# Optimization experiments

Hardware: AMD Instinct MI355X
Metric: run time of the kernel (lower is better)

The kernel has to match this reference:

```python
import jax, jax.numpy as jnp
import numpy as np

PAD_IDX = 1
BATCH = 16
TLEN = 128
SLEN = 400          # full source length
AGENDA_LEN = 100    # slen_ in src_map
CONTEXT_LEN = SLEN - AGENDA_LEN
INPUT_SIZE = 1024
VOCAB = 32000
CVOCAB = 120


def setup_inputs() -> dict:
    key = jax.random.key(0)
    k1, k2, k3, k4, k5, k6, k7 = jax.random.split(key, 7)
    N = BATCH * TLEN
    hidden = jax.random.normal(k1, (N, INPUT_SIZE), dtype=jnp.float32)
    attn = jax.random.uniform(k2, (N, SLEN), dtype=jnp.float32)
    attn = attn / jnp.sum(attn, axis=1, keepdims=True)  # attention-like rows
    src_map = jax.random.uniform(k3, (AGENDA_LEN, BATCH, CVOCAB), dtype=jnp.float32)
    W = jax.random.normal(k4, (VOCAB, INPUT_SIZE), dtype=jnp.float32) * 0.02
    b = jnp.zeros((VOCAB,), dtype=jnp.float32)
    W_copy = jax.random.normal(k5, (1, INPUT_SIZE), dtype=jnp.float32) * 0.02
    b_copy = jnp.zeros((1,), dtype=jnp.float32)
    return {"hidden": hidden, "attn": attn, "src_map": src_map,
            "W": W, "b": b, "W_copy": W_copy, "b_copy": b_copy}


def reference(hidden, attn, src_map, W, b, W_copy, b_copy):
    # hidden: (tlen*batch, d), attn: (tlen*batch, slen), src_map: (agenda, batch, cvocab)
    agenda_len, batch, cvocab = src_map.shape
    slen = attn.shape[1]
    context_len = slen - agenda_len

    logits = hidden @ W.T + b                       # (N, vocab)
    logits = logits.at[:, PAD_IDX].set(-jnp.inf)
    prob = jax.nn.softmax(logits, axis=1)
    p_copy = jax.nn.sigmoid(hidden @ W_copy.T + b_copy)  # (N, 1)

    out_prob = prob * (1.0 - p_copy)                # (N, vocab)
    mul_attn = attn[:, context_len:] * p_copy       # (N, agenda)

    # rows are ordered (tlen, batch); bmm against per-batch indicator map
    ma = mul_attn.reshape(-1, batch, agenda_len)    # (tlen, batch, agenda)
    copy_prob = jnp.einsum('tba,abv->tbv', ma, src_map)  # (tlen, batch, cvocab)
    copy_prob = copy_prob.reshape(-1, cvocab)       # (N, cvocab)

    return jnp.concatenate([out_prob, copy_prob], axis=1), p_copy
```

## Files before the change

### kernel.cpp

```cpp
#include <hip/hip_runtime.h>

#define M_DIM 2048
#define K_DIM 1024
#define N_DIM 32000
#define CVOCAB 120
#define AGENDA 100
#define SLEN 400
#define CTX 300
#define BATCH 16
#define OUT_STRIDE 32120
#define PAD_IDX 1

#define TM 256
#define TN 256
#define BK 64
#define BUFSZ (TM * BK)
#define NKT (K_DIM / BK)
#define MT (M_DIM / TM)
#define NT (N_DIM / TN)

typedef float f32x4_t  __attribute__((ext_vector_type(4)));
typedef __bf16 bf16x8_t __attribute__((ext_vector_type(8)));
typedef unsigned short u16x8_t __attribute__((ext_vector_type(8)));
typedef unsigned short u16x4_t __attribute__((ext_vector_type(4)));

__device__ __forceinline__ unsigned short f2bf(float f) {
    union { float f; unsigned int u; } c; c.f = f;
    unsigned int u = c.u;
    u += 0x7FFFu + ((u >> 16) & 1u);
    return (unsigned short)(u >> 16);
}

__device__ __forceinline__ unsigned short f2h(float f) {
    _Float16 h = (_Float16)f;
    unsigned short u; __builtin_memcpy(&u, &h, 2); return u;
}
__device__ __forceinline__ float h2f(unsigned short u) {
    _Float16 h; __builtin_memcpy(&h, &u, 2); return (float)h;
}

__device__ __forceinline__ void async_copy16(const void* gsrc, void* ldst) {
    __builtin_amdgcn_global_load_lds(
        (__attribute__((address_space(1))) unsigned int*)(gsrc),
        (__attribute__((address_space(3))) unsigned int*)(ldst),
        16, 0, 0);
}

__global__ void cast_bf16_kernel(const float4* __restrict__ W, const float4* __restrict__ H,
                                 unsigned short* __restrict__ Wb, unsigned short* __restrict__ Hb) {
    const size_t NW4 = (size_t)N_DIM * K_DIM / 4;
    const size_t NH4 = (size_t)M_DIM * K_DIM / 4;
    size_t idx = (size_t)blockIdx.x * 256 + threadIdx.x;
    float4 v; unsigned short* dst;
    if (idx < NW4)            { v = W[idx];        dst = Wb + idx * 4; }
    else if (idx < NW4 + NH4) { v = H[idx - NW4];  dst = Hb + (idx - NW4) * 4; }
    else return;
    u16x4_t o;
    o[0] = f2bf(v.x); o[1] = f2bf(v.y); o[2] = f2bf(v.z); o[3] = f2bf(v.w);
    *(u16x4_t*)dst = o;
}

__global__ void pcopy_kernel(const float* __restrict__ hidden, const float* __restrict__ Wc,
                             const float* __restrict__ bc, float* __restrict__ pcopy,
                             float* __restrict__ rowsum) {
    int row  = blockIdx.x * 4 + (threadIdx.x >> 6);
    int lane = threadIdx.x & 63;
    const float4* h = (const float4*)(hidden + (size_t)row * K_DIM);
    const float4* w = (const float4*)Wc;
    float s = 0.f;
    #pragma unroll
    for (int i = 0; i < 4; ++i) {
        float4 a = h[lane + 64 * i];
        float4 b = w[lane + 64 * i];
        s += a.x * b.x + a.y * b.y + a.z * b.z + a.w * b.w;
    }
    #pragma unroll
    for (int m = 1; m < 64; m <<= 1) s += __shfl_xor(s, m);
    if (lane == 0) {
        float p = 1.0f / (1.0f + __expf(-(s + bc[0])));
        pcopy[row] = p;
        rowsum[row] = 0.0f;
    }
}

__global__ __launch_bounds__(1024, 4) void gemm_exp_kernel(
    const unsigned short* __restrict__ A,
    const unsigned short* __restrict__ B,
    const float* __restrict__ bias,
    float* __restrict__ out,
    float* __restrict__ rowsum)
{
    __shared__ unsigned short sA[2][BUFSZ];
    __shared__ unsigned short sB[2][BUFSZ];
    __shared__ float sRow[TM];

    const int tid   = threadIdx.x;
    const int lane  = tid & 63;
    const int q     = lane >> 4;
    const int lr    = lane & 15;
    const int wv    = tid >> 6;
    const int waveM = wv >> 2;
    const int waveN = wv & 3;

    const int bid = blockIdx.x;
    const int t   = (bid & 7) * NT + (bid >> 3);
    const int rowBase = (t & 7) * TM;
    const int colBase = (t >> 3) * TN;

    f32x4_t acc[4][4] = {};
    if (tid < TM) sRow[tid] = 0.0f;

    const int p0 = tid,        m0 = p0 >> 3, j0 = (p0 & 7) ^ (m0 & 7);
    const int p1 = 1024 + tid, m1 = p1 >> 3, j1 = (p1 & 7) ^ (m1 & 7);
    const unsigned short* aSrc0 = A + (size_t)(rowBase + m0) * K_DIM + j0 * 8;
    const unsigned short* aSrc1 = A + (size_t)(rowBase + m1) * K_DIM + j1 * 8;
    const unsigned short* bSrc0 = B + (size_t)(colBase + m0) * K_DIM + j0 * 8;
    const unsigned short* bSrc1 = B + (size_t)(colBase + m1) * K_DIM + j1 * 8;
    const int dOff0 = (tid & ~63) * 8;
    const int dOff1 = (1024 + (tid & ~63)) * 8;

    async_copy16(aSrc0, &sA[0][dOff0]);
    async_copy16(aSrc1, &sA[0][dOff1]);
    async_copy16(bSrc0, &sB[0][dOff0]);
    async_copy16(bSrc1, &sB[0][dOff1]);
    __syncthreads();

    for (int kt = 0; kt < NKT; ++kt) {
        const int cur = kt & 1;
        if (kt + 1 < NKT) {
            const int nb = cur ^ 1;
            const int k0 = (kt + 1) * BK;
            async_copy16(aSrc0 + k0, &sA[nb][dOff0]);
            async_copy16(aSrc1 + k0, &sA[nb][dOff1]);
            async_copy16(bSrc0 + k0, &sB[nb][dOff0]);
            async_copy16(bSrc1 + k0, &sB[nb][dOff1]);
        }
        const unsigned short* pA = sA[cur];
        const unsigned short* pB = sB[cur];
        #pragma unroll
        for (int s = 0; s < 2; ++s) {
            u16x8_t af[4], bfr[4];
            #pragma unroll
            for (int r = 0; r < 4; ++r) {
                int m  = waveM * 64 + r * 16 + lr;
                int ch = (s * 4 + q) ^ (m & 7);
                af[r] = *(const u16x8_t*)(pA + m * BK + ch * 8);
            }
            #pragma unroll
            for (int c = 0; c < 4; ++c) {
                int n  = waveN * 64 + c * 16 + lr;
                int ch = (s * 4 + q) ^ (n & 7);
                bfr[c] = *(const u16x8_t*)(pB + n * BK + ch * 8);
            }
            #pragma unroll
            for (int r = 0; r < 4; ++r)
                #pragma unroll
                for (int c = 0; c < 4; ++c)
                    acc[r][c] = __builtin_amdgcn_mfma_f32_16x16x32_bf16(
                        __builtin_bit_cast(bf16x8_t, af[r]),
                        __builtin_bit_cast(bf16x8_t, bfr[c]),
                        acc[r][c], 0, 0, 0);
        }
        __syncthreads();
    }

    float bb[4];
    #pragma unroll
    for (int c = 0; c < 4; ++c) bb[c] = bias[colBase + waveN * 64 + c * 16 + lr];

    #pragma unroll
    for (int r = 0; r < 4; ++r) {
        float rsum[4] = {0.f, 0.f, 0.f, 0.f};
        #pragma unroll
        for (int c = 0; c < 4; ++c) {
            int gcol = colBase + waveN * 64 + c * 16 + lr;
            bool pad = (gcol == PAD_IDX);
            #pragma unroll
            for (int d = 0; d < 4; ++d) {
                int grow = rowBase + waveM * 64 + r * 16 + q * 4 + d;
                float e = pad ? 0.0f : __expf(acc[r][c][d] + bb[c]);
                ((unsigned short*)(out + (size_t)grow * OUT_STRIDE))[gcol] = f2h(e);
                rsum[d] += e;
            }
        }
        #pragma unroll
        for (int d = 0; d < 4; ++d) {
            float v = rsum[d];
            v += __shfl_xor(v, 1);
            v += __shfl_xor(v, 2);
            v += __shfl_xor(v, 4);
            v += __shfl_xor(v, 8);
            if (lr == 0) {
                int lrow = waveM * 64 + r * 16 + q * 4 + d;
                atomicAdd(&sRow[lrow], v);
            }
        }
    }
    __syncthreads();
    if (tid < TM) atomicAdd(&rowsum[rowBase + tid], sRow[tid]);
}

__global__ __launch_bounds__(512) void finalize_kernel(
    float* __restrict__ out, const float* __restrict__ rowsum,
    const float* __restrict__ pcopy, const float* __restrict__ attn,
    const float* __restrict__ src_map, float* __restrict__ out_tail) {
    const int n   = blockIdx.x;
    const int tid = threadIdx.x;
    __shared__ unsigned short sE[N_DIM];
    __shared__ float ma[AGENDA];

    const float p = pcopy[n];
    const float scale = (1.0f - p) / rowsum[n];

    const u16x8_t* src = (const u16x8_t*)(out + (size_t)n * OUT_STRIDE);
    for (int j = tid; j < N_DIM / 8; j += 512)
        *(u16x8_t*)(sE + j * 8) = src[j];
    if (tid < AGENDA) ma[tid] = attn[(size_t)n * SLEN + CTX + tid] * p;
    __syncthreads();

    float4* row4 = (float4*)(out + (size_t)n * OUT_STRIDE);
    for (int j = tid; j < N_DIM / 4; j += 512) {
        u16x4_t h = *(const u16x4_t*)(sE + j * 4);
        float4 v;
        v.x = h2f(h[0]) * scale;
        v.y = h2f(h[1]) * scale;
        v.z = h2f(h[2]) * scale;
        v.w = h2f(h[3]) * scale;
        row4[j] = v;
    }

    if (tid < CVOCAB) {
        int bidx = n & (BATCH - 1);
        float s = 0.f;
        #pragma unroll 4
        for (int a = 0; a < AGENDA; ++a)
            s += ma[a] * src_map[(size_t)(a * BATCH + bidx) * CVOCAB + tid];
        out[(size_t)n * OUT_STRIDE + N_DIM + tid] = s;
    }
    if (tid == 0) out_tail[n] = p;
}

extern "C" void kernel_launch(void* const* d_in, const int* in_sizes, int n_in,
                              void* d_out, int out_size, void* d_ws, size_t ws_size,
                              hipStream_t stream) {
    const float* hidden  = (const float*)d_in[0];
    const float* attn    = (const float*)d_in[1];
    const float* src_map = (const float*)d_in[2];
    const float* W       = (const float*)d_in[3];
    const float* b       = (const float*)d_in[4];
    const float* W_copy  = (const float*)d_in[5];
    const float* b_copy  = (const float*)d_in[6];
    float* out = (float*)d_out;

    char* ws = (char*)d_ws;
    unsigned short* Wb = (unsigned short*)ws;
    unsigned short* Hb = (unsigned short*)(ws + 65536000);
    float* rowsum      = (float*)(ws + 65536000 + 4194304);
    float* pcopy       = (float*)(ws + 65536000 + 4194304 + 8192);

    float* out_tail = out + (size_t)M_DIM * OUT_STRIDE;

    {
        size_t total4 = (size_t)N_DIM * K_DIM / 4 + (size_t)M_DIM * K_DIM / 4;
        int blocks = (int)((total4 + 255) / 256);
        cast_bf16_kernel<<<blocks, 256, 0, stream>>>((const float4*)W, (const float4*)hidden, Wb, Hb);
    }
    pcopy_kernel<<<M_DIM / 4, 256, 0, stream>>>(hidden, W_copy, b_copy, pcopy, rowsum);
    gemm_exp_kernel<<<MT * NT, 1024, 0, stream>>>(Hb, Wb, b, out, rowsum);
    finalize_kernel<<<M_DIM, 512, 0, stream>>>(out, rowsum, pcopy, attn, src_map, out_tail);
}
```

Before: 582.8 us.

## Restructure GEMM main loop into 8-wave ping-pong schedule with deeper prefetch

The GEMM block drops from 16 waves to 8. Each wave now computes a 128x64 sub-tile with 32 accumulators, which raises register reuse of the B fragments. The K loop is split into half-K stages across a 4-buffer LDS ring (128KB) with two-stage-ahead async prefetch. Explicit vmcnt waits, s_barrier phases, sched_barrier and setprio interleave the loads with the MFMA bursts. The larger LDS footprint and register pressure may limit occupancy to one block per CU, and the many barriers add synchronisation cost.

```diff
diff --git a/kernel.cpp b/kernel.cpp
--- a/kernel.cpp
+++ b/kernel.cpp
@@ -14,7 +14,6 @@
 #define TM 256
 #define TN 256
 #define BK 64
-#define BUFSZ (TM * BK)
 #define NKT (K_DIM / BK)
 #define MT (M_DIM / TM)
 #define NT (N_DIM / TN)
@@ -83,102 +82,135 @@
     }
 }
 
-__global__ __launch_bounds__(1024, 4) void gemm_exp_kernel(
+__global__ __launch_bounds__(512, 2) void gemm_exp_kernel(
     const unsigned short* __restrict__ A,
     const unsigned short* __restrict__ B,
     const float* __restrict__ bias,
     float* __restrict__ out,
     float* __restrict__ rowsum)
 {
-    __shared__ unsigned short sA[2][BUFSZ];
-    __shared__ unsigned short sB[2][BUFSZ];
+    __shared__ unsigned short lds[65536];
     __shared__ float sRow[TM];
 
-    const int tid   = threadIdx.x;
-    const int lane  = tid & 63;
-    const int q     = lane >> 4;
-    const int lr    = lane & 15;
-    const int wv    = tid >> 6;
-    const int waveM = wv >> 2;
-    const int waveN = wv & 3;
+    const int tid  = threadIdx.x;
+    const int lane = tid & 63;
+    const int q    = lane >> 4;
+    const int lr   = lane & 15;
+    const int wv   = tid >> 6;
+    const int wr   = wv >> 2;
+    const int wc   = wv & 3;
 
     const int bid = blockIdx.x;
-    const int t   = (bid & 7) * NT + (bid >> 3);
-    const int rowBase = (t & 7) * TM;
-    const int colBase = (t >> 3) * TN;
-
-    f32x4_t acc[4][4] = {};
+    const int t0  = (bid & 7) * NT + (bid >> 3);
+    const int rowBase = (t0 & 7) * TM;
+    const int colBase = (t0 >> 3) * TN;
+
     if (tid < TM) sRow[tid] = 0.0f;
 
-    const int p0 = tid,        m0 = p0 >> 3, j0 = (p0 & 7) ^ (m0 & 7);
-    const int p1 = 1024 + tid, m1 = p1 >> 3, j1 = (p1 & 7) ^ (m1 & 7);
-    const unsigned short* aSrc0 = A + (size_t)(rowBase + m0) * K_DIM + j0 * 8;
-    const unsigned short* aSrc1 = A + (size_t)(rowBase + m1) * K_DIM + j1 * 8;
-    const unsigned short* bSrc0 = B + (size_t)(colBase + m0) * K_DIM + j0 * 8;
-    const unsigned short* bSrc1 = B + (size_t)(colBase + m1) * K_DIM + j1 * 8;
-    const int dOff0 = (tid & ~63) * 8;
-    const int dOff1 = (1024 + (tid & ~63)) * 8;
-
-    async_copy16(aSrc0, &sA[0][dOff0]);
-    async_copy16(aSrc1, &sA[0][dOff1]);
-    async_copy16(bSrc0, &sB[0][dOff0]);
-    async_copy16(bSrc1, &sB[0][dOff1]);
-    __syncthreads();
-
-    for (int kt = 0; kt < NKT; ++kt) {
-        const int cur = kt & 1;
-        if (kt + 1 < NKT) {
-            const int nb = cur ^ 1;
-            const int k0 = (kt + 1) * BK;
-            async_copy16(aSrc0 + k0, &sA[nb][dOff0]);
-            async_copy16(aSrc1 + k0, &sA[nb][dOff1]);
-            async_copy16(bSrc0 + k0, &sB[nb][dOff0]);
-            async_copy16(bSrc1 + k0, &sB[nb][dOff1]);
-        }
-        const unsigned short* pA = sA[cur];
-        const unsigned short* pB = sB[cur];
-        #pragma unroll
-        for (int s = 0; s < 2; ++s) {
-            u16x8_t af[4], bfr[4];
-            #pragma unroll
-            for (int r = 0; r < 4; ++r) {
-                int m  = waveM * 64 + r * 16 + lr;
-                int ch = (s * 4 + q) ^ (m & 7);
-                af[r] = *(const u16x8_t*)(pA + m * BK + ch * 8);
-            }
-            #pragma unroll
-            for (int c = 0; c < 4; ++c) {
-                int n  = waveN * 64 + c * 16 + lr;
-                int ch = (s * 4 + q) ^ (n & 7);
-                bfr[c] = *(const u16x8_t*)(pB + n * BK + ch * 8);
-            }
-            #pragma unroll
-            for (int r = 0; r < 4; ++r)
-                #pragma unroll
-                for (int c = 0; c < 4; ++c)
-                    acc[r][c] = __builtin_amdgcn_mfma_f32_16x16x32_bf16(
-                        __builtin_bit_cast(bf16x8_t, af[r]),
-                        __builtin_bit_cast(bf16x8_t, bfr[c]),
-                        acc[r][c], 0, 0, 0);
-        }
-        __syncthreads();
-    }
+    const int mS0 = tid >> 2,         cS0 = tid & 3;
+    const int mS1 = (tid + 512) >> 2, cS1 = tid & 3;
+    const int jS0 = cS0 ^ ((mS0 >> 1) & 3);
+    const int jS1 = cS1 ^ ((mS1 >> 1) & 3);
+    const unsigned short* aS0 = A + (size_t)(rowBase + mS0) * K_DIM + jS0 * 8;
+    const unsigned short* aS1 = A + (size_t)(rowBase + mS1) * K_DIM + jS1 * 8;
+    const unsigned short* bS0 = B + (size_t)(colBase + mS0) * K_DIM + jS0 * 8;
+    const unsigned short* bS1 = B + (size_t)(colBase + mS1) * K_DIM + jS1 * 8;
+    const int dus0 = wv * 512;
+    const int dus1 = 4096 + wv * 512;
+
+    int aoff[8], boff[4];
+    #pragma unroll
+    for (int f = 0; f < 8; ++f) {
+        int m = wr * 128 + f * 16 + lr;
+        aoff[f] = m * 32 + ((q ^ ((m >> 1) & 3)) * 8);
+    }
+    #pragma unroll
+    for (int c = 0; c < 4; ++c) {
+        int n = wc * 64 + c * 16 + lr;
+        boff[c] = n * 32 + ((q ^ ((n >> 1) & 3)) * 8);
+    }
+
+    f32x4_t acc[8][4] = {};
+
+#define STAGE_A(TT, S) do {                                                  \
+    unsigned short* d_ = lds + (((TT) & 1) * 2 + (S)) * 8192;                \
+    const size_t ko_ = (size_t)(TT) * 64 + (S) * 32;                         \
+    async_copy16(aS0 + ko_, d_ + dus0);                                      \
+    async_copy16(aS1 + ko_, d_ + dus1); } while (0)
+
+#define STAGE_B(TT, S) do {                                                  \
+    unsigned short* d_ = lds + 32768 + (((TT) & 1) * 2 + (S)) * 8192;        \
+    const size_t ko_ = (size_t)(TT) * 64 + (S) * 32;                         \
+    async_copy16(bS0 + ko_, d_ + dus0);                                      \
+    async_copy16(bS1 + ko_, d_ + dus1); } while (0)
+
+    STAGE_A(0, 0); STAGE_B(0, 0);
+    STAGE_A(0, 1); STAGE_B(0, 1);
+    STAGE_A(1, 0); STAGE_B(1, 0);
+
+    #pragma unroll 1
+    for (int t = 0; t < NKT; ++t) {
+        const int p = t & 1;
+        if (t < NKT - 1) asm volatile("s_waitcnt vmcnt(4)" ::: "memory");
+        else             asm volatile("s_waitcnt vmcnt(0)" ::: "memory");
+        __builtin_amdgcn_s_barrier();
+        __builtin_amdgcn_sched_barrier(0);
+
+        u16x8_t bfv[4];
+
+#define PHASE(MH, S, STAGE_STMT) do {                                        \
+        const int sa_ = (p * 2 + (S)) * 8192;                                \
+        const int sb_ = 32768 + sa_;                                         \
+        u16x8_t af_[4];                                                      \
+        _Pragma("unroll")                                                    \
+        for (int r = 0; r < 4; ++r)                                          \
+            af_[r] = *(const u16x8_t*)(lds + sa_ + aoff[(MH) * 4 + r]);      \
+        if ((MH) == 0) {                                                     \
+            _Pragma("unroll")                                                \
+            for (int c = 0; c < 4; ++c)                                      \
+                bfv[c] = *(const u16x8_t*)(lds + sb_ + boff[c]);             \
+        }                                                                    \
+        STAGE_STMT;                                                          \
+        __builtin_amdgcn_sched_barrier(0);                                   \
+        __builtin_amdgcn_s_barrier();                                        \
+        __builtin_amdgcn_s_setprio(1);                                       \
+        _Pragma("unroll")                                                    \
+        for (int r = 0; r < 4; ++r) {                                        \
+            _Pragma("unroll")                                                \
+            for (int c = 0; c < 4; ++c)                                      \
+                acc[(MH) * 4 + r][c] = __builtin_amdgcn_mfma_f32_16x16x32_bf16( \
+                    __builtin_bit_cast(bf16x8_t, af_[r]),                    \
+                    __builtin_bit_cast(bf16x8_t, bfv[c]),                    \
+                    acc[(MH) * 4 + r][c], 0, 0, 0);                          \
+        }                                                                    \
+        __builtin_amdgcn_s_setprio(0);                                       \
+        __builtin_amdgcn_sched_barrier(0);                                   \
+        __builtin_amdgcn_s_barrier(); } while (0)
+
+        PHASE(0, 0, { if (t < NKT - 1) STAGE_A(t + 1, 1); });
+        PHASE(1, 0, { if (t < NKT - 1) STAGE_B(t + 1, 1); });
+        PHASE(0, 1, { if (t < NKT - 2) STAGE_A(t + 2, 0); });
+        PHASE(1, 1, { if (t < NKT - 2) STAGE_B(t + 2, 0); });
+#undef PHASE
+    }
+#undef STAGE_A
+#undef STAGE_B
 
     float bb[4];
     #pragma unroll
-    for (int c = 0; c < 4; ++c) bb[c] = bias[colBase + waveN * 64 + c * 16 + lr];
-
-    #pragma unroll
-    for (int r = 0; r < 4; ++r) {
+    for (int c = 0; c < 4; ++c) bb[c] = bias[colBase + wc * 64 + c * 16 + lr];
+
+    #pragma unroll
+    for (int f = 0; f < 8; ++f) {
         float rsum[4] = {0.f, 0.f, 0.f, 0.f};
         #pragma unroll
         for (int c = 0; c < 4; ++c) {
-            int gcol = colBase + waveN * 64 + c * 16 + lr;
+            int gcol = colBase + wc * 64 + c * 16 + lr;
             bool pad = (gcol == PAD_IDX);
             #pragma unroll
             for (int d = 0; d < 4; ++d) {
-                int grow = rowBase + waveM * 64 + r * 16 + q * 4 + d;
-                float e = pad ? 0.0f : __expf(acc[r][c][d] + bb[c]);
+                int grow = rowBase + wr * 128 + f * 16 + q * 4 + d;
+                float e = pad ? 0.0f : __expf(acc[f][c][d] + bb[c]);
                 ((unsigned short*)(out + (size_t)grow * OUT_STRIDE))[gcol] = f2h(e);
                 rsum[d] += e;
             }
@@ -191,7 +223,7 @@
             v += __shfl_xor(v, 4);
             v += __shfl_xor(v, 8);
             if (lr == 0) {
-                int lrow = waveM * 64 + r * 16 + q * 4 + d;
+                int lrow = wr * 128 + f * 16 + q * 4 + d;
                 atomicAdd(&sRow[lrow], v);
             }
         }
@@ -266,6 +298,6 @@
         cast_bf16_kernel<<<blocks, 256, 0, stream>>>((const float4*)W, (const float4*)hidden, Wb, Hb);
     }
     pcopy_kernel<<<M_DIM / 4, 256, 0, stream>>>(hidden, W_copy, b_copy, pcopy, rowsum);
-    gemm_exp_kernel<<<MT * NT, 1024, 0, stream>>>(Hb, Wb, b, out, rowsum);
+    gemm_exp_kernel<<<MT * NT, 512, 0, stream>>>(Hb, Wb, b, out, rowsum);
     finalize_kernel<<<M_DIM, 512, 0, stream>>>(out, rowsum, pcopy, attn, src_map, out_tail);
 }
```

Result: no change. 589.1 us (+1.1%).

## Stage exp values in workspace buffer and move copy-prob into pcopy kernel

Applied to the files above, without the earlier changes.

The GEMM epilogue now writes fp16 exp values to a separate, densely packed workspace buffer when the workspace is large enough. A plain streaming normalize kernel then reads that buffer and writes the fp32 output, so it no longer stages rows through shared memory the way the in-place version must. The copy-probability einsum and the p_copy tail write move into the p_copy kernel, and the cast kernel becomes a grid-stride loop over 2048 blocks. The cost is an extra 128MB workspace buffer, plus a fallback path that keeps the old in-place behaviour.

```diff
diff --git a/kernel.cpp b/kernel.cpp
--- a/kernel.cpp
+++ b/kernel.cpp
@@ -46,25 +46,31 @@
         16, 0, 0);
 }
 
-__global__ void cast_bf16_kernel(const float4* __restrict__ W, const float4* __restrict__ H,
-                                 unsigned short* __restrict__ Wb, unsigned short* __restrict__ Hb) {
+__global__ __launch_bounds__(256) void cast_bf16_kernel(
+    const float4* __restrict__ W, const float4* __restrict__ H,
+    unsigned short* __restrict__ Wb, unsigned short* __restrict__ Hb) {
     const size_t NW4 = (size_t)N_DIM * K_DIM / 4;
     const size_t NH4 = (size_t)M_DIM * K_DIM / 4;
-    size_t idx = (size_t)blockIdx.x * 256 + threadIdx.x;
-    float4 v; unsigned short* dst;
-    if (idx < NW4)            { v = W[idx];        dst = Wb + idx * 4; }
-    else if (idx < NW4 + NH4) { v = H[idx - NW4];  dst = Hb + (idx - NW4) * 4; }
-    else return;
-    u16x4_t o;
-    o[0] = f2bf(v.x); o[1] = f2bf(v.y); o[2] = f2bf(v.z); o[3] = f2bf(v.w);
-    *(u16x4_t*)dst = o;
-}
-
-__global__ void pcopy_kernel(const float* __restrict__ hidden, const float* __restrict__ Wc,
-                             const float* __restrict__ bc, float* __restrict__ pcopy,
-                             float* __restrict__ rowsum) {
-    int row  = blockIdx.x * 4 + (threadIdx.x >> 6);
-    int lane = threadIdx.x & 63;
+    const size_t total = NW4 + NH4;
+    const size_t stride = (size_t)gridDim.x * 256;
+    for (size_t idx = (size_t)blockIdx.x * 256 + threadIdx.x; idx < total; idx += stride) {
+        float4 v; unsigned short* dst;
+        if (idx < NW4) { v = W[idx];        dst = Wb + idx * 4; }
+        else           { v = H[idx - NW4];  dst = Hb + (idx - NW4) * 4; }
+        u16x4_t o;
+        o[0] = f2bf(v.x); o[1] = f2bf(v.y); o[2] = f2bf(v.z); o[3] = f2bf(v.w);
+        *(u16x4_t*)dst = o;
+    }
+}
+
+__global__ __launch_bounds__(256) void pcopy_copy_kernel(
+    const float* __restrict__ hidden, const float* __restrict__ Wc,
+    const float* __restrict__ bc, const float* __restrict__ attn,
+    const float* __restrict__ src_map,
+    float* __restrict__ out, float* __restrict__ out_tail,
+    float* __restrict__ pcopy, float* __restrict__ rowsum) {
+    const int row  = blockIdx.x * 4 + (threadIdx.x >> 6);
+    const int lane = threadIdx.x & 63;
     const float4* h = (const float4*)(hidden + (size_t)row * K_DIM);
     const float4* w = (const float4*)Wc;
     float s = 0.f;
@@ -76,18 +82,33 @@
     }
     #pragma unroll
     for (int m = 1; m < 64; m <<= 1) s += __shfl_xor(s, m);
+    const float p = 1.0f / (1.0f + __expf(-(s + bc[0])));
     if (lane == 0) {
-        float p = 1.0f / (1.0f + __expf(-(s + bc[0])));
-        pcopy[row] = p;
-        rowsum[row] = 0.0f;
-    }
+        pcopy[row]   = p;
+        out_tail[row] = p;
+        rowsum[row]  = 0.0f;
+    }
+    const int bidx = row & (BATCH - 1);
+    const float* arow = attn + (size_t)row * SLEN + CTX;
+    float s0 = 0.f, s1 = 0.f;
+    #pragma unroll 4
+    for (int a = 0; a < AGENDA; ++a) {
+        float m = arow[a];
+        const float* sm = src_map + (size_t)(a * BATCH + bidx) * CVOCAB;
+        s0 += m * sm[lane];
+        if (lane < CVOCAB - 64) s1 += m * sm[lane + 64];
+    }
+    float* orow = out + (size_t)row * OUT_STRIDE + N_DIM;
+    orow[lane] = s0 * p;
+    if (lane < CVOCAB - 64) orow[lane + 64] = s1 * p;
 }
 
 __global__ __launch_bounds__(1024, 4) void gemm_exp_kernel(
     const unsigned short* __restrict__ A,
     const unsigned short* __restrict__ B,
     const float* __restrict__ bias,
-    float* __restrict__ out,
+    unsigned short* __restrict__ E,
+    const size_t eStride,
     float* __restrict__ rowsum)
 {
     __shared__ unsigned short sA[2][BUFSZ];
@@ -179,7 +200,7 @@
             for (int d = 0; d < 4; ++d) {
                 int grow = rowBase + waveM * 64 + r * 16 + q * 4 + d;
                 float e = pad ? 0.0f : __expf(acc[r][c][d] + bb[c]);
-                ((unsigned short*)(out + (size_t)grow * OUT_STRIDE))[gcol] = f2h(e);
+                E[(size_t)grow * eStride + gcol] = f2h(e);
                 rsum[d] += e;
             }
         }
@@ -200,24 +221,37 @@
     if (tid < TM) atomicAdd(&rowsum[rowBase + tid], sRow[tid]);
 }
 
-__global__ __launch_bounds__(512) void finalize_kernel(
+__global__ __launch_bounds__(256) void normalize_kernel(
+    const unsigned short* __restrict__ E, float* __restrict__ out,
+    const float* __restrict__ rowsum, const float* __restrict__ pcopy) {
+    const int n   = blockIdx.x;
+    const int tid = threadIdx.x;
+    const float scale = (1.0f - pcopy[n]) / rowsum[n];
+    const u16x8_t* src = (const u16x8_t*)(E + (size_t)n * N_DIM);
+    float4* dst = (float4*)(out + (size_t)n * OUT_STRIDE);
+    for (int j = tid; j < N_DIM / 8; j += 256) {
+        u16x8_t h = src[j];
+        float4 a, b;
+        a.x = h2f(h[0]) * scale; a.y = h2f(h[1]) * scale;
+        a.z = h2f(h[2]) * scale; a.w = h2f(h[3]) * scale;
+        b.x = h2f(h[4]) * scale; b.y = h2f(h[5]) * scale;
+        b.z = h2f(h[6]) * scale; b.w = h2f(h[7]) * scale;
+        dst[j * 2]     = a;
+        dst[j * 2 + 1] = b;
+    }
+}
+
+__global__ __launch_bounds__(512) void normalize_inplace_kernel(
     float* __restrict__ out, const float* __restrict__ rowsum,
-    const float* __restrict__ pcopy, const float* __restrict__ attn,
-    const float* __restrict__ src_map, float* __restrict__ out_tail) {
+    const float* __restrict__ pcopy) {
     const int n   = blockIdx.x;
     const int tid = threadIdx.x;
     __shared__ unsigned short sE[N_DIM];
-    __shared__ float ma[AGENDA];
-
-    const float p = pcopy[n];
-    const float scale = (1.0f - p) / rowsum[n];
-
+    const float scale = (1.0f - pcopy[n]) / rowsum[n];
     const u16x8_t* src = (const u16x8_t*)(out + (size_t)n * OUT_STRIDE);
     for (int j = tid; j < N_DIM / 8; j += 512)
         *(u16x8_t*)(sE + j * 8) = src[j];
-    if (tid < AGENDA) ma[tid] = attn[(size_t)n * SLEN + CTX + tid] * p;
     __syncthreads();
-
     float4* row4 = (float4*)(out + (size_t)n * OUT_STRIDE);
     for (int j = tid; j < N_DIM / 4; j += 512) {
         u16x4_t h = *(const u16x4_t*)(sE + j * 4);
@@ -228,16 +262,6 @@
         v.w = h2f(h[3]) * scale;
         row4[j] = v;
     }
-
-    if (tid < CVOCAB) {
-        int bidx = n & (BATCH - 1);
-        float s = 0.f;
-        #pragma unroll 4
-        for (int a = 0; a < AGENDA; ++a)
-            s += ma[a] * src_map[(size_t)(a * BATCH + bidx) * CVOCAB + tid];
-        out[(size_t)n * OUT_STRIDE + N_DIM + tid] = s;
-    }
-    if (tid == 0) out_tail[n] = p;
 }
 
 extern "C" void kernel_launch(void* const* d_in, const int* in_sizes, int n_in,
@@ -257,15 +281,21 @@
     unsigned short* Hb = (unsigned short*)(ws + 65536000);
     float* rowsum      = (float*)(ws + 65536000 + 4194304);
     float* pcopy       = (float*)(ws + 65536000 + 4194304 + 8192);
+    unsigned short* E  = (unsigned short*)(ws + 65536000 + 4194304 + 16384);
+    const size_t wsNeeded = 65536000ull + 4194304 + 16384 + (size_t)M_DIM * N_DIM * 2;
+    const bool useWsE = (ws_size >= wsNeeded);
 
     float* out_tail = out + (size_t)M_DIM * OUT_STRIDE;
 
-    {
-        size_t total4 = (size_t)N_DIM * K_DIM / 4 + (size_t)M_DIM * K_DIM / 4;
-        int blocks = (int)((total4 + 255) / 256);
-        cast_bf16_kernel<<<blocks, 256, 0, stream>>>((const float4*)W, (const float4*)hidden, Wb, Hb);
-    }
-    pcopy_kernel<<<M_DIM / 4, 256, 0, stream>>>(hidden, W_copy, b_copy, pcopy, rowsum);
-    gemm_exp_kernel<<<MT * NT, 1024, 0, stream>>>(Hb, Wb, b, out, rowsum);
-    finalize_kernel<<<M_DIM, 512, 0, stream>>>(out, rowsum, pcopy, attn, src_map, out_tail);
-}
+    cast_bf16_kernel<<<2048, 256, 0, stream>>>((const float4*)W, (const float4*)hidden, Wb, Hb);
+    pcopy_copy_kernel<<<M_DIM / 4, 256, 0, stream>>>(hidden, W_copy, b_copy, attn, src_map,
+                                                     out, out_tail, pcopy, rowsum);
+    if (useWsE) {
+        gemm_exp_kernel<<<MT * NT, 1024, 0, stream>>>(Hb, Wb, b, E, (size_t)N_DIM, rowsum);
+        normalize_kernel<<<M_DIM, 256, 0, stream>>>(E, out, rowsum, pcopy);
+    } else {
+        gemm_exp_kernel<<<MT * NT, 1024, 0, stream>>>(Hb, Wb, b, (unsigned short*)out,
+                                                      (size_t)OUT_STRIDE * 2, rowsum);
+        normalize_inplace_kernel<<<M_DIM, 512, 0, stream>>>(out, rowsum, pcopy);
+    }
+}
```

New measurement: 640.4 us. 1.1x slower.
